# Performance work log

Measured on AMD Instinct MI355X. Metric: run time of the kernel, lower is better.

## Reference

```python
import jax, jax.numpy as jnp
import numpy as np

LN_EPS = 1e-5


def setup_inputs() -> dict:
    key = jax.random.key(0)
    ks = jax.random.split(key, 6)
    N, E, D = 100000, 600000, 128
    x = jax.random.normal(ks[0], (N, D), dtype=jnp.float32)
    edge_index = jax.random.randint(ks[1], (2, E), 0, N, dtype=jnp.int64)
    dropout_mask = jax.random.uniform(ks[2], (N, D), dtype=jnp.float32)
    ln_gamma = jnp.ones((D,), dtype=jnp.float32)
    ln_beta = jnp.zeros((D,), dtype=jnp.float32)
    W_l = jax.random.normal(ks[3], (D, D), dtype=jnp.float32) / np.sqrt(D)
    b_l = jnp.zeros((D,), dtype=jnp.float32)
    W_r = jax.random.normal(ks[4], (D, D), dtype=jnp.float32) / np.sqrt(D)
    return {"x": x, "edge_index": edge_index, "dropout_mask": dropout_mask,
            "ln_gamma": ln_gamma, "ln_beta": ln_beta,
            "W_l": W_l, "b_l": b_l, "W_r": W_r}


def reference(x, edge_index, dropout_mask, ln_gamma, ln_beta, W_l, b_l, W_r):
    N = x.shape[0]
    # LayerNorm (elementwise affine) -> ReLU -> dropout mask
    mu = jnp.mean(x, axis=-1, keepdims=True)
    var = jnp.mean(jnp.square(x - mu), axis=-1, keepdims=True)
    h = (x - mu) * jax.lax.rsqrt(var + LN_EPS) * ln_gamma + ln_beta
    h = jax.nn.relu(h) * dropout_mask  # [N, D]
    # SAGEConv with mean aggregation: messages flow src -> dst
    src, dst = edge_index[0], edge_index[1]
    agg = jax.ops.segment_sum(h[src], dst, num_segments=N)  # [N, D]
    cnt = jax.ops.segment_sum(jnp.ones_like(dst, dtype=h.dtype), dst,
                              num_segments=N)
    mean_agg = agg / jnp.maximum(cnt, 1.0)[:, None]
    # out = lin_l(mean_agg) + lin_r(h); PyG stores weights as [out, in]
    return mean_agg @ W_l.T + b_l + h @ W_r.T
```

## Files before the change

### kernel.cpp

```cpp
#include <hip/hip_runtime.h>

#define LN_EPS 1e-5f
#define D 128
#define SCAN_CHUNK 1024
#define LDSA_STRIDE 264

typedef __attribute__((ext_vector_type(4))) float f32x4;
typedef __attribute__((ext_vector_type(8))) short bf16x8;

static __device__ __forceinline__ ushort f2bf(float f) {
    union { float f; unsigned u; } a; a.f = f;
    unsigned r = a.u + 0x7FFF + ((a.u >> 16) & 1);
    return (ushort)(r >> 16);
}
static __device__ __forceinline__ float bf2f(ushort u) {
    union { unsigned u; float f; } a; a.u = ((unsigned)u) << 16;
    return a.f;
}

__global__ void prep_w(const float* __restrict__ Wl,
                       const float* __restrict__ Wr,
                       ushort* __restrict__ Bfrag,
                       int* __restrict__ hist,
                       int* __restrict__ csums, int N) {
    int t = blockIdx.x * blockDim.x + threadIdx.x;
    if (t < 8 * 8 * 64 * 8) {
        int i    = t & 7;
        int lane = (t >> 3) & 63;
        int jb   = (t >> 9) & 7;
        int ks   = t >> 12;
        int k = ks * 32 + (lane >> 4) * 8 + i;
        int j = jb * 16 + (lane & 15);
        float v = (k < D) ? Wl[j * D + k] : Wr[j * D + (k - D)];
        Bfrag[t] = f2bf(v);
    }
    if (t < 128) csums[t] = 0;
    for (int i = t; i < N; i += gridDim.x * blockDim.x) hist[i] = 0;
}

__global__ void hist_k(const int* __restrict__ ei, int* __restrict__ hist, int E) {
    int base = (blockIdx.x * blockDim.x + threadIdx.x) * 4;
    const int* dst = ei + E;
    if (base + 3 < E) {
        int4 d = *(const int4*)(dst + base);
        atomicAdd(&hist[d.x], 1);
        atomicAdd(&hist[d.y], 1);
        atomicAdd(&hist[d.z], 1);
        atomicAdd(&hist[d.w], 1);
    } else {
        for (int i = base; i < E && i < base + 4; i++) atomicAdd(&hist[dst[i]], 1);
    }
}

__global__ void scan_all(const int* __restrict__ hist, int* __restrict__ offs,
                         int* __restrict__ cursor, int* __restrict__ csums, int N) {
    __shared__ int lds[256];
    __shared__ int base_s;
    int base = blockIdx.x * SCAN_CHUNK;
    int t = threadIdx.x;
    int idx0 = base + t * 4;
    int v[4];
#pragma unroll
    for (int i = 0; i < 4; i++) {
        int idx = idx0 + i;
        v[i] = (idx < N) ? hist[idx] : 0;
    }
    lds[t] = v[0] + v[1] + v[2] + v[3];
    __syncthreads();
    for (int off = 1; off < 256; off <<= 1) {
        int add = (t >= off) ? lds[t - off] : 0;
        __syncthreads();
        lds[t] += add;
        __syncthreads();
    }
    int run = (t == 0) ? 0 : lds[t - 1];
    if (t == 255)
        __hip_atomic_store(&csums[blockIdx.x], lds[255] | 0x40000000,
                           __ATOMIC_RELEASE, __HIP_MEMORY_SCOPE_AGENT);
    if (t < 64) {
        int b = (int)blockIdx.x;
        int acc = 0;
        for (int c = t; c < b; c += 64) {
            int w;
            do {
                w = __hip_atomic_load(&csums[c], __ATOMIC_ACQUIRE,
                                      __HIP_MEMORY_SCOPE_AGENT);
            } while (!(w & 0x40000000));
            acc += w & 0x3FFFFFFF;
        }
#pragma unroll
        for (int off = 32; off > 0; off >>= 1) acc += __shfl_xor(acc, off);
        if (t == 0) base_s = acc;
    }
    __syncthreads();
    run += base_s;
#pragma unroll
    for (int i = 0; i < 4; i++) {
        int idx = idx0 + i;
        if (idx < N) {
            offs[idx] = run;
            cursor[idx] = run;
        }
        run += v[i];
    }
}

__global__ void ln_sort(const float* __restrict__ x,
                        const float* __restrict__ mask,
                        const float* __restrict__ gamma,
                        const float* __restrict__ beta,
                        ushort* __restrict__ hbf,
                        const int* __restrict__ ei,
                        int* __restrict__ cursor,
                        int* __restrict__ sorted_src,
                        int N, int E, int lnBlocks) {
    if ((int)blockIdx.x >= lnBlocks) {
        int e = ((int)blockIdx.x - lnBlocks) * (int)blockDim.x + (int)threadIdx.x;
        if (e < E) {
            int dst = ei[E + e];
            int pos = atomicAdd(&cursor[dst], 1);
            sorted_src[pos] = ei[e];
        }
        return;
    }
    int lane = threadIdx.x & 63;
    int wid  = ((int)blockIdx.x * (int)blockDim.x + (int)threadIdx.x) >> 6;
    int node = wid * 2 + (lane >> 5);
    if (node >= N) return;
    int sl = lane & 31;
    f32x4 v = ((const f32x4*)(x + (size_t)node * D))[sl];
    float s  = v.x + v.y + v.z + v.w;
    float ss = v.x * v.x + v.y * v.y + v.z * v.z + v.w * v.w;
#pragma unroll
    for (int off = 16; off > 0; off >>= 1) {
        s  += __shfl_xor(s, off);
        ss += __shfl_xor(ss, off);
    }
    float mu  = s * (1.0f / D);
    float var = ss * (1.0f / D) - mu * mu;
    float rs  = rsqrtf(var + LN_EPS);
    f32x4 g = ((const f32x4*)gamma)[sl];
    f32x4 b = ((const f32x4*)beta)[sl];
    f32x4 m = ((const f32x4*)(mask + (size_t)node * D))[sl];
    ushort4 o;
    o.x = f2bf(fmaxf((v.x - mu) * rs * g.x + b.x, 0.0f) * m.x);
    o.y = f2bf(fmaxf((v.y - mu) * rs * g.y + b.y, 0.0f) * m.y);
    o.z = f2bf(fmaxf((v.z - mu) * rs * g.z + b.z, 0.0f) * m.z);
    o.w = f2bf(fmaxf((v.w - mu) * rs * g.w + b.w, 0.0f) * m.w);
    ((ushort4*)(hbf + (size_t)node * D))[sl] = o;
}

__global__ void __launch_bounds__(256, 4)
agg_gemm(float* __restrict__ out,
         const ushort* __restrict__ hbf,
         const int* __restrict__ sorted_src,
         const int* __restrict__ offs,
         const int* __restrict__ hist,
         const ushort* __restrict__ Bfrag,
         const float* __restrict__ bl,
         int N, int E) {
    __shared__ ushort Alds[64 * LDSA_STRIDE];
    int tid  = threadIdx.x;
    int wave = tid >> 6;
    int lane = tid & 63;
    int n0 = blockIdx.x * 64;

#pragma unroll
    for (int it = 0; it < 4; it++) {
        int chunk = tid + 256 * it;
        int row = chunk >> 4;
        int c8  = chunk & 15;
        int node = n0 + row;
        bf16x8 vh = (bf16x8){0,0,0,0,0,0,0,0};
        if (node < N) vh = *(const bf16x8*)(hbf + (size_t)node * D + c8 * 8);
        *(bf16x8*)&Alds[row * LDSA_STRIDE + 128 + c8 * 8] = vh;
    }

    int g  = lane >> 4;
    int sl = lane & 15;
    int row0 = wave * 16 + g;
    int start[4], deg[4], dm1[4];
#pragma unroll
    for (int p = 0; p < 4; p++) {
        int node = n0 + row0 + p * 4;
        start[p] = 0; deg[p] = 0;
        if (node < N) { start[p] = offs[node]; deg[p] = hist[node]; }
        dm1[p] = deg[p] - 1; if (dm1[p] < 0) dm1[p] = 0;
    }
    float acc[4][8];
#pragma unroll
    for (int p = 0; p < 4; p++)
#pragma unroll
        for (int q = 0; q < 8; q++) acc[p][q] = 0.0f;

    int dmax = max(max(deg[0], deg[1]), max(deg[2], deg[3]));
    int Em = E - 1;
    int ia[4], ib[4];
#pragma unroll
    for (int p = 0; p < 4; p++) {
        int pa = start[p];                         if (pa > Em) pa = Em;
        int j1 = (1 < dm1[p]) ? 1 : dm1[p];
        int pb = start[p] + j1;                    if (pb > Em) pb = Em;
        ia[p] = sorted_src[pa];
        ib[p] = sorted_src[pb];
    }
    for (int j = 0; j < dmax; j += 2) {
        int ca[4], cb[4];
#pragma unroll
        for (int p = 0; p < 4; p++) { ca[p] = ia[p]; cb[p] = ib[p]; }
#pragma unroll
        for (int p = 0; p < 4; p++) {
            int j2 = (j + 2 < dm1[p]) ? j + 2 : dm1[p];
            int j3 = (j + 3 < dm1[p]) ? j + 3 : dm1[p];
            int pa = start[p] + j2; if (pa > Em) pa = Em;
            int pb = start[p] + j3; if (pb > Em) pb = Em;
            ia[p] = sorted_src[pa];
            ib[p] = sorted_src[pb];
        }
#pragma unroll
        for (int p = 0; p < 4; p++) {
            bf16x8 v = *(const bf16x8*)(hbf + (size_t)ca[p] * D + sl * 8);
            float m = (j < deg[p]) ? 1.0f : 0.0f;
#pragma unroll
            for (int q = 0; q < 8; q++) acc[p][q] += bf2f((ushort)v[q]) * m;
        }
#pragma unroll
        for (int p = 0; p < 4; p++) {
            bf16x8 v = *(const bf16x8*)(hbf + (size_t)cb[p] * D + sl * 8);
            float m = (j + 1 < deg[p]) ? 1.0f : 0.0f;
#pragma unroll
            for (int q = 0; q < 8; q++) acc[p][q] += bf2f((ushort)v[q]) * m;
        }
    }
#pragma unroll
    for (int p = 0; p < 4; p++) {
        float inv = 1.0f / fmaxf((float)deg[p], 1.0f);
        bf16x8 o;
#pragma unroll
        for (int q = 0; q < 8; q++) o[q] = (short)f2bf(acc[p][q] * inv);
        *(bf16x8*)&Alds[(row0 + p * 4) * LDSA_STRIDE + sl * 8] = o;
    }
    __syncthreads();

    bf16x8 breg[8][2];
#pragma unroll
    for (int ks = 0; ks < 8; ks++)
#pragma unroll
        for (int jj = 0; jj < 2; jj++) {
            int jb = wave * 2 + jj;
            breg[ks][jj] = *(const bf16x8*)(Bfrag + (size_t)((ks * 8 + jb) * 64 + lane) * 8);
        }

    f32x4 acc2[4][2];
#pragma unroll
    for (int nb = 0; nb < 4; nb++)
#pragma unroll
        for (int jj = 0; jj < 2; jj++)
            acc2[nb][jj] = (f32x4){0.f, 0.f, 0.f, 0.f};

    int arow = lane & 15;
    int akoff = (lane >> 4) * 8;
#pragma unroll
    for (int ks = 0; ks < 8; ks++) {
#pragma unroll
        for (int nb = 0; nb < 4; nb++) {
            bf16x8 a = *(const bf16x8*)&Alds[(nb * 16 + arow) * LDSA_STRIDE + ks * 32 + akoff];
            acc2[nb][0] = __builtin_amdgcn_mfma_f32_16x16x32_bf16(a, breg[ks][0], acc2[nb][0], 0, 0, 0);
            acc2[nb][1] = __builtin_amdgcn_mfma_f32_16x16x32_bf16(a, breg[ks][1], acc2[nb][1], 0, 0, 0);
        }
    }

    float bias0 = bl[wave * 32 + (lane & 15)];
    float bias1 = bl[wave * 32 + 16 + (lane & 15)];
    int rbase = (lane >> 4) * 4;
#pragma unroll
    for (int nb = 0; nb < 4; nb++) {
#pragma unroll
        for (int r = 0; r < 4; r++) {
            int row = nb * 16 + rbase + r;
            if (n0 + row < N) {
                float* orow = out + (size_t)(n0 + row) * D + wave * 32 + (lane & 15);
                orow[0]  = acc2[nb][0][r] + bias0;
                orow[16] = acc2[nb][1][r] + bias1;
            }
        }
    }
}

extern "C" void kernel_launch(void* const* d_in, const int* in_sizes, int n_in,
                              void* d_out, int out_size, void* d_ws, size_t ws_size,
                              hipStream_t stream) {
    const float* x     = (const float*)d_in[0];
    const int*   ei    = (const int*)  d_in[1];
    const float* mask  = (const float*)d_in[2];
    const float* gamma = (const float*)d_in[3];
    const float* beta  = (const float*)d_in[4];
    const float* Wl    = (const float*)d_in[5];
    const float* bl    = (const float*)d_in[6];
    const float* Wr    = (const float*)d_in[7];
    float* out = (float*)d_out;

    int N = in_sizes[0] / D;
    int E = in_sizes[1] / 2;
    int chunks = (N + SCAN_CHUNK - 1) / SCAN_CHUNK;

    ushort* hbf   = (ushort*)d_ws;
    ushort* Bfrag = hbf + (size_t)N * D;
    int* hist   = (int*)(Bfrag + 32768);
    int* offs   = hist + N;
    int* cursor = offs + N;
    int* csums  = cursor + N;
    int* ssrc   = csums + 128;

    int lnBlocks   = (N + 7) / 8;
    int sortBlocks = (E + 255) / 256;

    prep_w<<<512, 256, 0, stream>>>(Wl, Wr, Bfrag, hist, csums, N);
    hist_k<<<(E / 4 + 255) / 256, 256, 0, stream>>>(ei, hist, E);
    scan_all<<<chunks, 256, 0, stream>>>(hist, offs, cursor, csums, N);
    ln_sort<<<lnBlocks + sortBlocks, 256, 0, stream>>>(x, mask, gamma, beta, hbf,
                                                       ei, cursor, ssrc, N, E, lnBlocks);
    agg_gemm<<<(N + 63) / 64, 256, 0, stream>>>(out, hbf, ssrc, offs, hist, Bfrag,
                                                bl, N, E);
}
```

Before: 256.9 us.

## Fuse LayerNorm with histogram, split edge sort, deepen gather prefetch to four

LayerNorm now runs in the same launch as the destination histogram rather than alongside the edge scatter, and each 16-lane group handles one node with 8 elements per lane. The scatter into sorted order becomes its own small kernel after the scan. The aggregation loop now prefetches four neighbour indices per row instead of two, which gives more loads in flight at the cost of more registers. The aim is to balance the launch stages better and hide gather latency.

```diff
diff --git a/kernel.cpp b/kernel.cpp
--- a/kernel.cpp
+++ b/kernel.cpp
@@ -38,18 +38,71 @@
     for (int i = t; i < N; i += gridDim.x * blockDim.x) hist[i] = 0;
 }
 
-__global__ void hist_k(const int* __restrict__ ei, int* __restrict__ hist, int E) {
-    int base = (blockIdx.x * blockDim.x + threadIdx.x) * 4;
-    const int* dst = ei + E;
-    if (base + 3 < E) {
-        int4 d = *(const int4*)(dst + base);
-        atomicAdd(&hist[d.x], 1);
-        atomicAdd(&hist[d.y], 1);
-        atomicAdd(&hist[d.z], 1);
-        atomicAdd(&hist[d.w], 1);
-    } else {
-        for (int i = base; i < E && i < base + 4; i++) atomicAdd(&hist[dst[i]], 1);
-    }
+__global__ void ln_hist(const float* __restrict__ x,
+                        const float* __restrict__ mask,
+                        const float* __restrict__ gamma,
+                        const float* __restrict__ beta,
+                        ushort* __restrict__ hbf,
+                        const int* __restrict__ ei,
+                        int* __restrict__ hist,
+                        int N, int E, int lnBlocks) {
+    if ((int)blockIdx.x >= lnBlocks) {
+        int base = (((int)blockIdx.x - lnBlocks) * 256 + (int)threadIdx.x) * 4;
+        const int* dst = ei + E;
+        if (base + 3 < E) {
+            int4 d = *(const int4*)(dst + base);
+            atomicAdd(&hist[d.x], 1);
+            atomicAdd(&hist[d.y], 1);
+            atomicAdd(&hist[d.z], 1);
+            atomicAdd(&hist[d.w], 1);
+        } else {
+            for (int i = base; i < E && i < base + 4; i++)
+                atomicAdd(&hist[dst[i]], 1);
+        }
+        return;
+    }
+    int tid  = threadIdx.x;
+    int lane = tid & 63;
+    int wid  = ((int)blockIdx.x * 256 + tid) >> 6;
+    int g2   = lane >> 4;
+    int sl   = lane & 15;
+    int node = wid * 4 + g2;
+    if (node >= N) return;
+
+    const float* xr = x + (size_t)node * D + sl * 8;
+    f32x4 v0 = *(const f32x4*)xr;
+    f32x4 v1 = *(const f32x4*)(xr + 4);
+    const float* mr = mask + (size_t)node * D + sl * 8;
+    f32x4 m0 = *(const f32x4*)mr;
+    f32x4 m1 = *(const f32x4*)(mr + 4);
+
+    float s  = (v0.x + v0.y) + (v0.z + v0.w) + (v1.x + v1.y) + (v1.z + v1.w);
+    float ss = (v0.x * v0.x + v0.y * v0.y) + (v0.z * v0.z + v0.w * v0.w)
+             + (v1.x * v1.x + v1.y * v1.y) + (v1.z * v1.z + v1.w * v1.w);
+#pragma unroll
+    for (int off = 8; off > 0; off >>= 1) {
+        s  += __shfl_xor(s, off);
+        ss += __shfl_xor(ss, off);
+    }
+    float mu  = s * (1.0f / D);
+    float var = ss * (1.0f / D) - mu * mu;
+    float rs  = rsqrtf(var + LN_EPS);
+
+    f32x4 g0 = *(const f32x4*)(gamma + sl * 8);
+    f32x4 g1 = *(const f32x4*)(gamma + sl * 8 + 4);
+    f32x4 b0 = *(const f32x4*)(beta + sl * 8);
+    f32x4 b1 = *(const f32x4*)(beta + sl * 8 + 4);
+
+    bf16x8 o;
+    o[0] = (short)f2bf(fmaxf((v0.x - mu) * rs * g0.x + b0.x, 0.0f) * m0.x);
+    o[1] = (short)f2bf(fmaxf((v0.y - mu) * rs * g0.y + b0.y, 0.0f) * m0.y);
+    o[2] = (short)f2bf(fmaxf((v0.z - mu) * rs * g0.z + b0.z, 0.0f) * m0.z);
+    o[3] = (short)f2bf(fmaxf((v0.w - mu) * rs * g0.w + b0.w, 0.0f) * m0.w);
+    o[4] = (short)f2bf(fmaxf((v1.x - mu) * rs * g1.x + b1.x, 0.0f) * m1.x);
+    o[5] = (short)f2bf(fmaxf((v1.y - mu) * rs * g1.y + b1.y, 0.0f) * m1.y);
+    o[6] = (short)f2bf(fmaxf((v1.z - mu) * rs * g1.z + b1.z, 0.0f) * m1.z);
+    o[7] = (short)f2bf(fmaxf((v1.w - mu) * rs * g1.w + b1.w, 0.0f) * m1.w);
+    *(bf16x8*)(hbf + (size_t)node * D + sl * 8) = o;
 }
 
 __global__ void scan_all(const int* __restrict__ hist, int* __restrict__ offs,
@@ -78,9 +131,8 @@
         __hip_atomic_store(&csums[blockIdx.x], lds[255] | 0x40000000,
                            __ATOMIC_RELEASE, __HIP_MEMORY_SCOPE_AGENT);
     if (t < 64) {
-        int b = (int)blockIdx.x;
         int acc = 0;
-        for (int c = t; c < b; c += 64) {
+        for (int c = t; c < (int)blockIdx.x; c += 64) {
             int w;
             do {
                 w = __hip_atomic_load(&csums[c], __ATOMIC_ACQUIRE,
@@ -105,49 +157,13 @@
     }
 }
 
-__global__ void ln_sort(const float* __restrict__ x,
-                        const float* __restrict__ mask,
-                        const float* __restrict__ gamma,
-                        const float* __restrict__ beta,
-                        ushort* __restrict__ hbf,
-                        const int* __restrict__ ei,
-                        int* __restrict__ cursor,
-                        int* __restrict__ sorted_src,
-                        int N, int E, int lnBlocks) {
-    if ((int)blockIdx.x >= lnBlocks) {
-        int e = ((int)blockIdx.x - lnBlocks) * (int)blockDim.x + (int)threadIdx.x;
-        if (e < E) {
-            int dst = ei[E + e];
-            int pos = atomicAdd(&cursor[dst], 1);
-            sorted_src[pos] = ei[e];
-        }
-        return;
-    }
-    int lane = threadIdx.x & 63;
-    int wid  = ((int)blockIdx.x * (int)blockDim.x + (int)threadIdx.x) >> 6;
-    int node = wid * 2 + (lane >> 5);
-    if (node >= N) return;
-    int sl = lane & 31;
-    f32x4 v = ((const f32x4*)(x + (size_t)node * D))[sl];
-    float s  = v.x + v.y + v.z + v.w;
-    float ss = v.x * v.x + v.y * v.y + v.z * v.z + v.w * v.w;
-#pragma unroll
-    for (int off = 16; off > 0; off >>= 1) {
-        s  += __shfl_xor(s, off);
-        ss += __shfl_xor(ss, off);
-    }
-    float mu  = s * (1.0f / D);
-    float var = ss * (1.0f / D) - mu * mu;
-    float rs  = rsqrtf(var + LN_EPS);
-    f32x4 g = ((const f32x4*)gamma)[sl];
-    f32x4 b = ((const f32x4*)beta)[sl];
-    f32x4 m = ((const f32x4*)(mask + (size_t)node * D))[sl];
-    ushort4 o;
-    o.x = f2bf(fmaxf((v.x - mu) * rs * g.x + b.x, 0.0f) * m.x);
-    o.y = f2bf(fmaxf((v.y - mu) * rs * g.y + b.y, 0.0f) * m.y);
-    o.z = f2bf(fmaxf((v.z - mu) * rs * g.z + b.z, 0.0f) * m.z);
-    o.w = f2bf(fmaxf((v.w - mu) * rs * g.w + b.w, 0.0f) * m.w);
-    ((ushort4*)(hbf + (size_t)node * D))[sl] = o;
+__global__ void sort_edges(const int* __restrict__ ei, int* __restrict__ cursor,
+                           int* __restrict__ sorted_src, int E) {
+    int e = blockIdx.x * blockDim.x + threadIdx.x;
+    if (e >= E) return;
+    int dst = ei[E + e];
+    int pos = atomicAdd(&cursor[dst], 1);
+    sorted_src[pos] = ei[e];
 }
 
 __global__ void __launch_bounds__(256, 4)
@@ -195,41 +211,38 @@
 
     int dmax = max(max(deg[0], deg[1]), max(deg[2], deg[3]));
     int Em = E - 1;
-    int ia[4], ib[4];
-#pragma unroll
-    for (int p = 0; p < 4; p++) {
-        int pa = start[p];                         if (pa > Em) pa = Em;
-        int j1 = (1 < dm1[p]) ? 1 : dm1[p];
-        int pb = start[p] + j1;                    if (pb > Em) pb = Em;
-        ia[p] = sorted_src[pa];
-        ib[p] = sorted_src[pb];
-    }
-    for (int j = 0; j < dmax; j += 2) {
-        int ca[4], cb[4];
-#pragma unroll
-        for (int p = 0; p < 4; p++) { ca[p] = ia[p]; cb[p] = ib[p]; }
+    int idx[4][4];
+#pragma unroll
+    for (int k = 0; k < 4; k++)
 #pragma unroll
         for (int p = 0; p < 4; p++) {
-            int j2 = (j + 2 < dm1[p]) ? j + 2 : dm1[p];
-            int j3 = (j + 3 < dm1[p]) ? j + 3 : dm1[p];
-            int pa = start[p] + j2; if (pa > Em) pa = Em;
-            int pb = start[p] + j3; if (pb > Em) pb = Em;
-            ia[p] = sorted_src[pa];
-            ib[p] = sorted_src[pb];
-        }
-#pragma unroll
-        for (int p = 0; p < 4; p++) {
-            bf16x8 v = *(const bf16x8*)(hbf + (size_t)ca[p] * D + sl * 8);
-            float m = (j < deg[p]) ? 1.0f : 0.0f;
-#pragma unroll
-            for (int q = 0; q < 8; q++) acc[p][q] += bf2f((ushort)v[q]) * m;
-        }
-#pragma unroll
-        for (int p = 0; p < 4; p++) {
-            bf16x8 v = *(const bf16x8*)(hbf + (size_t)cb[p] * D + sl * 8);
-            float m = (j + 1 < deg[p]) ? 1.0f : 0.0f;
-#pragma unroll
-            for (int q = 0; q < 8; q++) acc[p][q] += bf2f((ushort)v[q]) * m;
+            int jc = (k < dm1[p]) ? k : dm1[p];
+            int pos = start[p] + jc; if (pos > Em) pos = Em;
+            idx[k][p] = sorted_src[pos];
+        }
+    for (int j = 0; j < dmax; j += 4) {
+        int cur[4][4];
+#pragma unroll
+        for (int k = 0; k < 4; k++)
+#pragma unroll
+            for (int p = 0; p < 4; p++) cur[k][p] = idx[k][p];
+#pragma unroll
+        for (int k = 0; k < 4; k++)
+#pragma unroll
+            for (int p = 0; p < 4; p++) {
+                int jn = j + 4 + k; jn = (jn < dm1[p]) ? jn : dm1[p];
+                int pos = start[p] + jn; if (pos > Em) pos = Em;
+                idx[k][p] = sorted_src[pos];
+            }
+#pragma unroll
+        for (int k = 0; k < 4; k++) {
+#pragma unroll
+            for (int p = 0; p < 4; p++) {
+                bf16x8 v = *(const bf16x8*)(hbf + (size_t)cur[k][p] * D + sl * 8);
+                float m = (j + k < deg[p]) ? 1.0f : 0.0f;
+#pragma unroll
+                for (int q = 0; q < 8; q++) acc[p][q] += bf2f((ushort)v[q]) * m;
+            }
         }
     }
 #pragma unroll
@@ -312,14 +325,14 @@
     int* csums  = cursor + N;
     int* ssrc   = csums + 128;
 
-    int lnBlocks   = (N + 7) / 8;
-    int sortBlocks = (E + 255) / 256;
+    int lnBlocks   = (N + 15) / 16;
+    int histBlocks = (E + 1023) / 1024;
 
     prep_w<<<512, 256, 0, stream>>>(Wl, Wr, Bfrag, hist, csums, N);
-    hist_k<<<(E / 4 + 255) / 256, 256, 0, stream>>>(ei, hist, E);
+    ln_hist<<<lnBlocks + histBlocks, 256, 0, stream>>>(x, mask, gamma, beta, hbf,
+                                                       ei, hist, N, E, lnBlocks);
     scan_all<<<chunks, 256, 0, stream>>>(hist, offs, cursor, csums, N);
-    ln_sort<<<lnBlocks + sortBlocks, 256, 0, stream>>>(x, mask, gamma, beta, hbf,
-                                                       ei, cursor, ssrc, N, E, lnBlocks);
+    sort_edges<<<(E + 255) / 256, 256, 0, stream>>>(ei, cursor, ssrc, E);
     agg_gemm<<<(N + 63) / 64, 256, 0, stream>>>(out, hbf, ssrc, offs, hist, Bfrag,
                                                 bl, N, E);
 }
```

Result: slower. 297.0 us (+15.6%).
